# Performance work log

Hardware: AMD Instinct MI355X
Metric: run time of the kernel (lower is better)

The kernel has to match this reference:

```python
import jax, jax.numpy as jnp
import numpy as np

B, W, H, C = 64, 32, 32, 64
K = 4096  # embedding_length


def setup_inputs() -> dict:
    key = jax.random.key(0)
    k1, k2 = jax.random.split(key)
    encoded = jax.random.normal(k1, (B, W, H, C), dtype=jnp.float32)
    # tf.random.uniform init in the original
    codebook = jax.random.uniform(k2, (K, C), dtype=jnp.float32)
    return {"encoded": encoded, "codebook": codebook}


def reference(encoded, codebook):
    b, w, h, c = encoded.shape
    x = encoded.reshape(b * w * h, c)  # [N, c]
    # the tiled tf.pow(x - e, 2).sum(-1), without the [N, K, c] intermediate).
    x_sq = jnp.sum(x * x, axis=-1, keepdims=True)          # [N, 1]
    e_sq = jnp.sum(codebook * codebook, axis=-1)           # [K]
    dist = x_sq - 2.0 * (x @ codebook.T) + e_sq[None, :]   # [N, K]
    idx = jnp.argmin(dist, axis=-1)                        # [N]
    q = codebook[idx].reshape(b, w, h, c)                  # gather
    # Straight-through estimator as in the original forward
    out = encoded + jax.lax.stop_gradient(q - encoded)
    return out, idx.reshape(b, w, h)
```

## Files before the change

kernel.cpp:

```cpp
#include <hip/hip_runtime.h>


#define NPTS    65536
#define CDIM    64
#define KCODES  4096
#define WAVES   4
#define KPW     (KCODES / WAVES)
#define TILES   (KPW / 16)
#define PADC    64
#define LISTCAP 4096
#define DELTA   0.25f

typedef __attribute__((ext_vector_type(8))) short short8;
typedef __attribute__((ext_vector_type(4))) float f32x4;

__device__ __forceinline__ unsigned short f2bf(float x) {
    unsigned u = __float_as_uint(x);
    return (unsigned short)((u + 0x7FFFu + ((u >> 16) & 1u)) >> 16);
}

struct BT { short8 b0, b1; };

__global__ __launch_bounds__(256) void vq_prep(const float* __restrict__ cb,
                                               short* __restrict__ cbb,
                                               float* __restrict__ h) {
    int k = blockIdx.x * 256 + threadIdx.x;
    const float4* p = reinterpret_cast<const float4*>(cb + (size_t)k * CDIM);
    float s0 = 0.f, s1 = 0.f, s2 = 0.f, s3 = 0.f;
#pragma unroll
    for (int i = 0; i < 16; i += 2) {
        float4 va = p[i], vb = p[i + 1];
        s0 = fmaf(va.x, va.x, s0); s1 = fmaf(va.y, va.y, s1);
        s2 = fmaf(va.z, va.z, s2); s3 = fmaf(va.w, va.w, s3);
        s0 = fmaf(vb.x, vb.x, s0); s1 = fmaf(vb.y, vb.y, s1);
        s2 = fmaf(vb.z, vb.z, s2); s3 = fmaf(vb.w, vb.w, s3);
        short8 o;
        o[0] = (short)f2bf(va.x); o[1] = (short)f2bf(va.y);
        o[2] = (short)f2bf(va.z); o[3] = (short)f2bf(va.w);
        o[4] = (short)f2bf(vb.x); o[5] = (short)f2bf(vb.y);
        o[6] = (short)f2bf(vb.z); o[7] = (short)f2bf(vb.w);
        *reinterpret_cast<short8*>(cbb + (size_t)k * CDIM + i * 4) = o;
    }
    h[k] = 0.5f * ((s0 + s1) + (s2 + s3));
}

__global__ __launch_bounds__(256) void vq_main(const float* __restrict__ enc,
                                               const float* __restrict__ cbf,
                                               const short* __restrict__ cbb,
                                               const float* __restrict__ h,
                                               float* __restrict__ out) {
    __shared__ unsigned list[LISTCAP];
    __shared__ float hlds[KCODES + PADC];
    __shared__ float rowmax[WAVES][64];
    __shared__ float thrL[64];
    __shared__ unsigned long long mkey[64];
    __shared__ unsigned lcnt;

    const int tid  = threadIdx.x;
    const int wid  = tid >> 6, lane = tid & 63;
    const int lrow = lane & 15, lseg = lane >> 4;
    const int pbase = blockIdx.x * 64;
    const int k0 = wid * KPW;

    if (tid == 0) lcnt = 0;
    if (tid < 64) mkey[tid] = ~0ull;
    for (int i = tid; i < KCODES + PADC; i += 256) hlds[i] = h[i];

    short8 afr[4][2];
#pragma unroll
    for (int rt = 0; rt < 4; ++rt)
#pragma unroll
        for (int kk = 0; kk < 2; ++kk) {
            const float4* xp = reinterpret_cast<const float4*>(
                enc + (size_t)(pbase + rt * 16 + lrow) * CDIM + kk * 32 + lseg * 8);
            float4 v0 = xp[0], v1 = xp[1];
            short8 a;
            a[0] = (short)f2bf(v0.x); a[1] = (short)f2bf(v0.y);
            a[2] = (short)f2bf(v0.z); a[3] = (short)f2bf(v0.w);
            a[4] = (short)f2bf(v1.x); a[5] = (short)f2bf(v1.y);
            a[6] = (short)f2bf(v1.z); a[7] = (short)f2bf(v1.w);
            afr[rt][kk] = a;
        }
    __syncthreads();

    auto loadB = [&](int ct, BT& s) {
        int code = k0 + ct * 16 + lrow;
        const short* base = cbb + (size_t)code * CDIM + lseg * 8;
        s.b0 = *reinterpret_cast<const short8*>(base);
        s.b1 = *reinterpret_cast<const short8*>(base + 32);
    };

    f32x4 best[4];
#pragma unroll
    for (int rt = 0; rt < 4; ++rt)
#pragma unroll
        for (int i = 0; i < 4; ++i) best[rt][i] = -__builtin_inff();

    {
        BT s0, s1, s2, s3;
        loadB(0, s0); loadB(8, s1); loadB(16, s2); loadB(24, s3);
#define SSBODY(SLOT, J)                                                        \
        {                                                                      \
            float nh = -hlds[k0 + (J) * 128 + lrow];                           \
            f32x4 acc[4];                                                      \
            _Pragma("unroll")                                                  \
            for (int rt = 0; rt < 4; ++rt) {                                   \
                acc[rt][0] = nh; acc[rt][1] = nh;                              \
                acc[rt][2] = nh; acc[rt][3] = nh;                              \
            }                                                                  \
            _Pragma("unroll")                                                  \
            for (int rt = 0; rt < 4; ++rt)                                     \
                acc[rt] = __builtin_amdgcn_mfma_f32_16x16x32_bf16(afr[rt][0], SLOT.b0, acc[rt], 0, 0, 0); \
            _Pragma("unroll")                                                  \
            for (int rt = 0; rt < 4; ++rt)                                     \
                acc[rt] = __builtin_amdgcn_mfma_f32_16x16x32_bf16(afr[rt][1], SLOT.b1, acc[rt], 0, 0, 0); \
            _Pragma("unroll")                                                  \
            for (int rt = 0; rt < 4; ++rt)                                     \
                _Pragma("unroll")                                              \
                for (int i = 0; i < 4; ++i)                                    \
                    best[rt][i] = fmaxf(best[rt][i], acc[rt][i]);              \
            loadB((((J) + 4) & 7) * 8, SLOT);                                  \
        }
        SSBODY(s0, 0) SSBODY(s1, 1) SSBODY(s2, 2) SSBODY(s3, 3)
        SSBODY(s0, 4) SSBODY(s1, 5) SSBODY(s2, 6) SSBODY(s3, 7)
#undef SSBODY
    }

#pragma unroll
    for (int m = 1; m <= 8; m <<= 1)
#pragma unroll
        for (int rt = 0; rt < 4; ++rt)
#pragma unroll
            for (int i = 0; i < 4; ++i)
                best[rt][i] = fmaxf(best[rt][i], __shfl_xor(best[rt][i], m, 64));
    if (lrow == 0) {
#pragma unroll
        for (int rt = 0; rt < 4; ++rt)
#pragma unroll
            for (int i = 0; i < 4; ++i)
                rowmax[wid][rt * 16 + lseg * 4 + i] = best[rt][i];
    }
    __syncthreads();
    if (tid < 64) {
        float m0 = fmaxf(rowmax[0][tid], rowmax[1][tid]);
        float m1 = fmaxf(rowmax[2][tid], rowmax[3][tid]);
        thrL[tid] = fmaxf(m0, m1) - DELTA;
    }
    __syncthreads();

    f32x4 mthr[4];
#pragma unroll
    for (int rt = 0; rt < 4; ++rt)
#pragma unroll
        for (int i = 0; i < 4; ++i) mthr[rt][i] = -thrL[rt * 16 + lseg * 4 + i];

    {
        BT s0, s1, s2, s3;
        loadB(0, s0); loadB(1, s1); loadB(2, s2); loadB(3, s3);
#define S2BODY(SLOT, T)                                                        \
        {                                                                      \
            float hh = hlds[k0 + (T) * 16 + lrow];                             \
            f32x4 acc[4];                                                      \
            _Pragma("unroll")                                                  \
            for (int rt = 0; rt < 4; ++rt)                                     \
                acc[rt] = __builtin_amdgcn_mfma_f32_16x16x32_bf16(afr[rt][0], SLOT.b0, mthr[rt], 0, 0, 0); \
            _Pragma("unroll")                                                  \
            for (int rt = 0; rt < 4; ++rt)                                     \
                acc[rt] = __builtin_amdgcn_mfma_f32_16x16x32_bf16(afr[rt][1], SLOT.b1, acc[rt], 0, 0, 0); \
            unsigned mask = 0u;                                                \
            _Pragma("unroll")                                                  \
            for (int rt = 0; rt < 4; ++rt)                                     \
                _Pragma("unroll")                                              \
                for (int i = 0; i < 4; ++i)                                    \
                    mask |= (acc[rt][i] >= hh) ? (1u << (rt * 4 + i)) : 0u;    \
            if (mask) {                                                        \
                unsigned code = (unsigned)(k0 + (T) * 16 + lrow);              \
                do {                                                           \
                    int kz = __builtin_ctz(mask);                              \
                    mask &= mask - 1u;                                         \
                    unsigned row = ((unsigned)(kz >> 2) << 4)                  \
                                 + (unsigned)(lseg * 4) + (unsigned)(kz & 3);   \
                    unsigned pos = atomicAdd(&lcnt, 1u);                       \
                    if (pos < LISTCAP) list[pos] = (row << 12) | code;         \
                } while (mask);                                                \
            }                                                                  \
            loadB((T) + 4, SLOT);           \
        }
        for (int t = 0; t < TILES; t += 4) {
            S2BODY(s0, t + 0)
            S2BODY(s1, t + 1)
            S2BODY(s2, t + 2)
            S2BODY(s3, t + 3)
        }
#undef S2BODY
    }
    __syncthreads();

    unsigned cnt = lcnt; if (cnt > LISTCAP) cnt = LISTCAP;
    for (unsigned t4 = tid; t4 < cnt * 4; t4 += 256) {
        unsigned t = t4 >> 2; int q = t4 & 3;
        unsigned e = list[t];
        int row = (int)(e >> 12), c = (int)(e & 4095u);
        const float4* xp = reinterpret_cast<const float4*>(enc + (size_t)(pbase + row) * CDIM) + q * 4;
        const float4* ep = reinterpret_cast<const float4*>(cbf + (size_t)c * CDIM) + q * 4;
        float a0 = 0.f, a1 = 0.f, a2 = 0.f, a3 = 0.f;
#pragma unroll
        for (int i = 0; i < 4; ++i) {
            float4 xv = xp[i], ev = ep[i];
            a0 = fmaf(xv.x, ev.x, a0); a1 = fmaf(xv.y, ev.y, a1);
            a2 = fmaf(xv.z, ev.z, a2); a3 = fmaf(xv.w, ev.w, a3);
        }
        float p = (a0 + a1) + (a2 + a3);
        p += __shfl_xor(p, 1, 64);
        p += __shfl_xor(p, 2, 64);
        if (q == 0) {
            float d2 = fmaf(-2.f, p, 2.f * hlds[c]);
            unsigned bb = __float_as_uint(d2);
            unsigned ord = bb ^ (unsigned)(((int)bb >> 31) | 0x80000000);
            atomicMin(&mkey[row], ((unsigned long long)ord << 32) | (unsigned)c);
        }
    }
    __syncthreads();

    {
        int p = tid >> 2, q = tid & 3;
        int c = (int)(mkey[p] & 4095u);
        const float4* ep = reinterpret_cast<const float4*>(cbf + (size_t)c * CDIM) + q * 4;
        float4* op = reinterpret_cast<float4*>(out + (size_t)(pbase + p) * CDIM) + q * 4;
#pragma unroll
        for (int i = 0; i < 4; ++i) op[i] = ep[i];
        if (tid < 64)
            out[(size_t)NPTS * CDIM + pbase + tid] = (float)(mkey[tid] & 4095u);
    }
}

extern "C" void kernel_launch(void* const* d_in, const int* in_sizes, int n_in,
                              void* d_out, int out_size, void* d_ws, size_t ws_size,
                              hipStream_t stream) {
    const float* enc = (const float*)d_in[0];
    const float* cb  = (const float*)d_in[1];
    float* out = (float*)d_out;

    short* cbb = (short*)d_ws;
    float* hws = (float*)(cbb + (size_t)(KCODES + PADC) * CDIM);

    vq_prep<<<KCODES / 256, 256, 0, stream>>>(cb, cbb, hws);
    vq_main<<<NPTS / 64, 256, 0, stream>>>(enc, cb, cbb, hws, out);
}
```

Before: 129.3 us.

## Halve points per block to raise occupancy and shrink register use

Each block now handles 32 points instead of 64, which halves the per-wave A fragments, accumulators and prefetch slots. The candidate list shrinks and launch bounds now request 8 blocks per SM, aiming for more resident waves to hide latency. In exchange, every codebook tile loaded from global/L2 is reused across only half as many points, doubling total B traffic and the per-block hlds load. The smaller LISTCAP also raises the risk of overflow dropping candidates.

```diff
diff --git a/kernel.cpp b/kernel.cpp
--- a/kernel.cpp
+++ b/kernel.cpp
@@ -5,10 +5,11 @@
 #define CDIM    64
 #define KCODES  4096
 #define WAVES   4
+#define PPB     32
 #define KPW     (KCODES / WAVES)
 #define TILES   (KPW / 16)
 #define PADC    64
-#define LISTCAP 4096
+#define LISTCAP 1536
 #define DELTA   0.25f
 
 typedef __attribute__((ext_vector_type(8))) short short8;
@@ -44,31 +45,31 @@
     h[k] = 0.5f * ((s0 + s1) + (s2 + s3));
 }
 
-__global__ __launch_bounds__(256) void vq_main(const float* __restrict__ enc,
-                                               const float* __restrict__ cbf,
-                                               const short* __restrict__ cbb,
-                                               const float* __restrict__ h,
-                                               float* __restrict__ out) {
+__global__ __launch_bounds__(256, 8) void vq_main(const float* __restrict__ enc,
+                                                  const float* __restrict__ cbf,
+                                                  const short* __restrict__ cbb,
+                                                  const float* __restrict__ h,
+                                                  float* __restrict__ out) {
     __shared__ unsigned list[LISTCAP];
     __shared__ float hlds[KCODES + PADC];
-    __shared__ float rowmax[WAVES][64];
-    __shared__ float thrL[64];
-    __shared__ unsigned long long mkey[64];
+    __shared__ float rowmax[WAVES][PPB];
+    __shared__ float thrL[PPB];
+    __shared__ unsigned long long mkey[PPB];
     __shared__ unsigned lcnt;
 
     const int tid  = threadIdx.x;
     const int wid  = tid >> 6, lane = tid & 63;
     const int lrow = lane & 15, lseg = lane >> 4;
-    const int pbase = blockIdx.x * 64;
+    const int pbase = blockIdx.x * PPB;
     const int k0 = wid * KPW;
 
     if (tid == 0) lcnt = 0;
-    if (tid < 64) mkey[tid] = ~0ull;
+    if (tid < PPB) mkey[tid] = ~0ull;
     for (int i = tid; i < KCODES + PADC; i += 256) hlds[i] = h[i];
 
-    short8 afr[4][2];
-#pragma unroll
-    for (int rt = 0; rt < 4; ++rt)
+    short8 afr[2][2];
+#pragma unroll
+    for (int rt = 0; rt < 2; ++rt)
 #pragma unroll
         for (int kk = 0; kk < 2; ++kk) {
             const float4* xp = reinterpret_cast<const float4*>(
@@ -90,86 +91,88 @@
         s.b1 = *reinterpret_cast<const short8*>(base + 32);
     };
 
-    f32x4 best[4];
-#pragma unroll
-    for (int rt = 0; rt < 4; ++rt)
+    f32x4 best[2];
+#pragma unroll
+    for (int rt = 0; rt < 2; ++rt)
 #pragma unroll
         for (int i = 0; i < 4; ++i) best[rt][i] = -__builtin_inff();
 
     {
-        BT s0, s1, s2, s3;
-        loadB(0, s0); loadB(8, s1); loadB(16, s2); loadB(24, s3);
+        BT s0, s1;
+        loadB(0, s0); loadB(8, s1);
 #define SSBODY(SLOT, J)                                                        \
         {                                                                      \
             float nh = -hlds[k0 + (J) * 128 + lrow];                           \
-            f32x4 acc[4];                                                      \
-            _Pragma("unroll")                                                  \
-            for (int rt = 0; rt < 4; ++rt) {                                   \
+            f32x4 acc[2];                                                      \
+            _Pragma("unroll")                                                  \
+            for (int rt = 0; rt < 2; ++rt) {                                   \
                 acc[rt][0] = nh; acc[rt][1] = nh;                              \
                 acc[rt][2] = nh; acc[rt][3] = nh;                              \
             }                                                                  \
             _Pragma("unroll")                                                  \
-            for (int rt = 0; rt < 4; ++rt)                                     \
+            for (int rt = 0; rt < 2; ++rt)                                     \
                 acc[rt] = __builtin_amdgcn_mfma_f32_16x16x32_bf16(afr[rt][0], SLOT.b0, acc[rt], 0, 0, 0); \
             _Pragma("unroll")                                                  \
-            for (int rt = 0; rt < 4; ++rt)                                     \
+            for (int rt = 0; rt < 2; ++rt)                                     \
                 acc[rt] = __builtin_amdgcn_mfma_f32_16x16x32_bf16(afr[rt][1], SLOT.b1, acc[rt], 0, 0, 0); \
             _Pragma("unroll")                                                  \
-            for (int rt = 0; rt < 4; ++rt)                                     \
+            for (int rt = 0; rt < 2; ++rt)                                     \
                 _Pragma("unroll")                                              \
                 for (int i = 0; i < 4; ++i)                                    \
                     best[rt][i] = fmaxf(best[rt][i], acc[rt][i]);              \
-            loadB((((J) + 4) & 7) * 8, SLOT);                                  \
-        }
-        SSBODY(s0, 0) SSBODY(s1, 1) SSBODY(s2, 2) SSBODY(s3, 3)
-        SSBODY(s0, 4) SSBODY(s1, 5) SSBODY(s2, 6) SSBODY(s3, 7)
+            loadB((((J) + 2) & 7) * 8, SLOT);                                  \
+        }
+        SSBODY(s0, 0) SSBODY(s1, 1)
+        SSBODY(s0, 2) SSBODY(s1, 3)
+        SSBODY(s0, 4) SSBODY(s1, 5)
+        SSBODY(s0, 6) SSBODY(s1, 7)
 #undef SSBODY
     }
 
 #pragma unroll
     for (int m = 1; m <= 8; m <<= 1)
 #pragma unroll
-        for (int rt = 0; rt < 4; ++rt)
+        for (int rt = 0; rt < 2; ++rt)
 #pragma unroll
             for (int i = 0; i < 4; ++i)
                 best[rt][i] = fmaxf(best[rt][i], __shfl_xor(best[rt][i], m, 64));
     if (lrow == 0) {
 #pragma unroll
-        for (int rt = 0; rt < 4; ++rt)
+        for (int rt = 0; rt < 2; ++rt)
 #pragma unroll
             for (int i = 0; i < 4; ++i)
                 rowmax[wid][rt * 16 + lseg * 4 + i] = best[rt][i];
     }
     __syncthreads();
-    if (tid < 64) {
+    if (tid < PPB) {
         float m0 = fmaxf(rowmax[0][tid], rowmax[1][tid]);
         float m1 = fmaxf(rowmax[2][tid], rowmax[3][tid]);
         thrL[tid] = fmaxf(m0, m1) - DELTA;
     }
     __syncthreads();
 
-    f32x4 mthr[4];
-#pragma unroll
-    for (int rt = 0; rt < 4; ++rt)
+    f32x4 mthr[2];
+#pragma unroll
+    for (int rt = 0; rt < 2; ++rt)
 #pragma unroll
         for (int i = 0; i < 4; ++i) mthr[rt][i] = -thrL[rt * 16 + lseg * 4 + i];
 
     {
-        BT s0, s1, s2, s3;
-        loadB(0, s0); loadB(1, s1); loadB(2, s2); loadB(3, s3);
+        BT s0, s1;
+        loadB(0, s0); loadB(1, s1);
 #define S2BODY(SLOT, T)                                                        \
         {                                                                      \
             float hh = hlds[k0 + (T) * 16 + lrow];                             \
-            f32x4 acc[4];                                                      \
-            _Pragma("unroll")                                                  \
-            for (int rt = 0; rt < 4; ++rt)                                     \
+            f32x4 acc[2];                                                      \
+            _Pragma("unroll")                                                  \
+            for (int rt = 0; rt < 2; ++rt)                                     \
                 acc[rt] = __builtin_amdgcn_mfma_f32_16x16x32_bf16(afr[rt][0], SLOT.b0, mthr[rt], 0, 0, 0); \
             _Pragma("unroll")                                                  \
-            for (int rt = 0; rt < 4; ++rt)                                     \
+            for (int rt = 0; rt < 2; ++rt)                                     \
                 acc[rt] = __builtin_amdgcn_mfma_f32_16x16x32_bf16(afr[rt][1], SLOT.b1, acc[rt], 0, 0, 0); \
             unsigned mask = 0u;                                                \
             _Pragma("unroll")                                                  \
-            for (int rt = 0; rt < 4; ++rt)                                     \
+            for (int rt = 0; rt < 2; ++rt)                                     \
                 _Pragma("unroll")                                              \
                 for (int i = 0; i < 4; ++i)                                    \
                     mask |= (acc[rt][i] >= hh) ? (1u << (rt * 4 + i)) : 0u;    \
@@ -184,13 +187,11 @@
                     if (pos < LISTCAP) list[pos] = (row << 12) | code;         \
                 } while (mask);                                                \
             }                                                                  \
-            loadB((T) + 4, SLOT);           \
-        }
-        for (int t = 0; t < TILES; t += 4) {
+            loadB((T) + 2, SLOT);           \
+        }
+        for (int t = 0; t < TILES; t += 2) {
             S2BODY(s0, t + 0)
             S2BODY(s1, t + 1)
-            S2BODY(s2, t + 2)
-            S2BODY(s3, t + 3)
         }
 #undef S2BODY
     }
@@ -223,13 +224,13 @@
     __syncthreads();
 
     {
-        int p = tid >> 2, q = tid & 3;
+        int p = tid >> 3, q = tid & 7;
         int c = (int)(mkey[p] & 4095u);
-        const float4* ep = reinterpret_cast<const float4*>(cbf + (size_t)c * CDIM) + q * 4;
-        float4* op = reinterpret_cast<float4*>(out + (size_t)(pbase + p) * CDIM) + q * 4;
-#pragma unroll
-        for (int i = 0; i < 4; ++i) op[i] = ep[i];
-        if (tid < 64)
+        const float4* ep = reinterpret_cast<const float4*>(cbf + (size_t)c * CDIM);
+        float4* op = reinterpret_cast<float4*>(out + (size_t)(pbase + p) * CDIM);
+        op[q] = ep[q];
+        op[q + 8] = ep[q + 8];
+        if (tid < PPB)
             out[(size_t)NPTS * CDIM + pbase + tid] = (float)(mkey[tid] & 4095u);
     }
 }
@@ -245,5 +246,5 @@
     float* hws = (float*)(cbb + (size_t)(KCODES + PADC) * CDIM);
 
     vq_prep<<<KCODES / 256, 256, 0, stream>>>(cb, cbb, hws);
-    vq_main<<<NPTS / 64, 256, 0, stream>>>(enc, cb, cbb, hws, out);
-}
+    vq_main<<<NPTS / PPB, 256, 0, stream>>>(enc, cb, cbb, hws, out);
+}
```

Result: slower. 172.1 us (+33.1%).
